# Performance work log

Hardware: AMD Instinct MI355X
Metric: run time of the kernel (lower is better)

## Reference

```python
import jax, jax.numpy as jnp
import numpy as np

N_NODES = 50000
N_EDGES = 1600000
D = 64            # gin_hidden_units == embedding_dim
N_GRAPHS = 512
N_CLASSES = 53
ITERS = 3
VOCAB = 3100
BN_EPS = 1e-5


def setup_inputs() -> dict:
    key = jax.random.key(0)
    ks = jax.random.split(key, 16)
    pkt_length = jax.random.randint(ks[0], (N_NODES,), 0, VOCAB, dtype=jnp.int32)
    src = jax.random.randint(ks[1], (N_EDGES,), 0, N_NODES, dtype=jnp.int32)
    dst = jax.random.randint(ks[2], (N_EDGES,), 0, N_NODES, dtype=jnp.int32)
    graph_ids = jnp.sort(jax.random.randint(ks[3], (N_NODES,), 0, N_GRAPHS, dtype=jnp.int32))
    s = 0.05
    emb = jax.random.normal(ks[4], (VOCAB, D), dtype=jnp.float32) * s
    eps = jnp.zeros((), dtype=jnp.float32)  # GINConv learn_eps init 0
    W1 = jax.random.normal(ks[5], (D, D), dtype=jnp.float32) * s
    b1 = jnp.zeros((D,), dtype=jnp.float32)
    W2 = jax.random.normal(ks[6], (D, D), dtype=jnp.float32) * s
    b2 = jnp.zeros((D,), dtype=jnp.float32)
    W3 = jax.random.normal(ks[7], (D, D), dtype=jnp.float32) * s
    b3 = jnp.zeros((D,), dtype=jnp.float32)
    gamma = jnp.ones((D,), dtype=jnp.float32)
    beta = jnp.zeros((D,), dtype=jnp.float32)
    Wc = jax.random.normal(ks[8], (ITERS * D, N_CLASSES), dtype=jnp.float32) * s
    bc = jnp.zeros((N_CLASSES,), dtype=jnp.float32)
    return {"pkt_length": pkt_length, "src": src, "dst": dst, "graph_ids": graph_ids,
            "emb": emb, "eps": eps, "W1": W1, "b1": b1, "W2": W2, "b2": b2,
            "W3": W3, "b3": b3, "gamma": gamma, "beta": beta, "Wc": Wc, "bc": bc}


def _mlp_bn(x, W1, b1, W2, b2, W3, b3, gamma, beta):
    # 3 Linear+ReLU layers, then BatchNorm1d (training-mode batch stats)
    x = jax.nn.relu(x @ W1 + b1)
    x = jax.nn.relu(x @ W2 + b2)
    x = jax.nn.relu(x @ W3 + b3)
    mean = jnp.mean(x, axis=0)
    var = jnp.var(x, axis=0)
    return gamma * (x - mean) * jax.lax.rsqrt(var + BN_EPS) + beta


def reference(pkt_length, src, dst, graph_ids, emb, eps, W1, b1, W2, b2, W3, b3, gamma, beta, Wc, bc):
    # node features via embedding lookup
    h = emb[pkt_length]  # [N, D]
    pooled = []
    for _ in range(ITERS):
        # GIN sum aggregation: agg[v] = sum_{(u->v)} h[u]
        agg = jax.ops.segment_sum(h[src], dst, num_segments=N_NODES)
        h = _mlp_bn((1.0 + eps) * h + agg, W1, b1, W2, b2, W3, b3, gamma, beta)
        # graph sum pooling
        pooled.append(jax.ops.segment_sum(h, graph_ids, num_segments=N_GRAPHS))
    graph_features = jnp.concatenate(pooled, axis=-1)  # [G, 3*D]
    return graph_features @ Wc + bc  # [G, nb_classes]
```

## Files before the change

### kernel.cpp

```cpp
#include <hip/hip_runtime.h>

#define N_NODES   50000
#define N_EDGES   1600000
#define DDIM      64
#define N_GRAPHS  512
#define N_CLASSES 53
#define ITERS     3
#define NB        782
#define NBLK      391
#define PPITCH    400
#define NPB       128
#define CHUNK     ((N_EDGES + NPB - 1) / NPB)
#define NZERO     (NB + N_GRAPHS)

typedef __bf16 bf16x8 __attribute__((ext_vector_type(8)));
typedef __bf16 bf16x4 __attribute__((ext_vector_type(4)));
typedef float  f32x4  __attribute__((ext_vector_type(4)));

__device__ __forceinline__ float blo16(unsigned w) { return __uint_as_float(w << 16); }
__device__ __forceinline__ float bhi16(unsigned w) { return __uint_as_float(w & 0xffff0000u); }

__global__ void embed_kernel(const int* __restrict__ pkt, const float4* __restrict__ emb,
                             bf16x4* __restrict__ hb4, int* __restrict__ zreg,
                             float* __restrict__ gmbt_id) {
  if (blockIdx.x == 0) {
    for (int i = threadIdx.x; i < NZERO; i += 256) zreg[i] = 0;
    if (threadIdx.x < 128) gmbt_id[threadIdx.x] = (threadIdx.x < 64) ? 1.0f : 0.0f;
  }
  int idx = blockIdx.x * 256 + threadIdx.x;
  if (idx >= N_NODES * 16) return;
  int node = idx >> 4;
  float4 v = emb[(size_t)pkt[node] * 16 + (idx & 15)];
  bf16x4 o;
  o[0] = (__bf16)v.x; o[1] = (__bf16)v.y; o[2] = (__bf16)v.z; o[3] = (__bf16)v.w;
  hb4[idx] = o;
}

__global__ void bucket_hist_kernel(const int* __restrict__ dst, int* __restrict__ bhist) {
  __shared__ int lh[NB];
  for (int i = threadIdx.x; i < NB; i += 256) lh[i] = 0;
  __syncthreads();
  int stride = gridDim.x * 256;
  for (int e = blockIdx.x * 256 + threadIdx.x; e < N_EDGES; e += stride)
    atomicAdd(&lh[dst[e] >> 6], 1);
  __syncthreads();
  for (int i = threadIdx.x; i < NB; i += 256)
    if (lh[i]) atomicAdd(&bhist[i], lh[i]);
}

__global__ void hist_kernel(const int* __restrict__ idx, int* __restrict__ counts, int n) {
  int i = blockIdx.x * 256 + threadIdx.x;
  if (i < n) atomicAdd(&counts[idx[i]], 1);
}

__device__ void scan_body(const int* __restrict__ counts, int* __restrict__ offs,
                          int* __restrict__ cursor, int n) {
  __shared__ int wsum[16];
  __shared__ int carry;
  int tid = threadIdx.x;
  if (tid == 0) carry = 0;
  __syncthreads();
  for (int base = 0; base < n; base += 1024) {
    int i = base + tid;
    int v = (i < n) ? counts[i] : 0;
    int x = v;
    #pragma unroll
    for (int off = 1; off < 64; off <<= 1) {
      int y = __shfl_up(x, off);
      if ((tid & 63) >= off) x += y;
    }
    int w = tid >> 6;
    if ((tid & 63) == 63) wsum[w] = x;
    __syncthreads();
    int woff = 0;
    for (int k = 0; k < w; ++k) woff += wsum[k];
    int incl = x + woff + carry;
    if (i < n) {
      offs[i] = incl - v;
      if (cursor) cursor[i] = incl - v;
    }
    __syncthreads();
    if (tid == 1023) carry = incl;
    __syncthreads();
  }
  if (tid == 0) offs[n] = carry;
}

__global__ void scans_kernel(const int* __restrict__ bhist, int* __restrict__ boffs,
                             int* __restrict__ bcursor, const int* __restrict__ gcnt,
                             int* __restrict__ goff) {
  if (blockIdx.x == 0) scan_body(bhist, boffs, bcursor, NB);
  else                 scan_body(gcnt, goff, nullptr, N_GRAPHS);
}

__global__ __launch_bounds__(1024) void partition_kernel(
    const int* __restrict__ src, const int* __restrict__ dst,
    int* __restrict__ bcursor, unsigned* __restrict__ ebuf) {
  __shared__ int lh[NB];
  __shared__ int lbase[NB];
  for (int i = threadIdx.x; i < NB; i += 1024) lh[i] = 0;
  __syncthreads();
  int e0 = blockIdx.x * CHUNK;
  int e1 = min(e0 + CHUNK, N_EDGES);
  for (int e = e0 + (int)threadIdx.x; e < e1; e += 1024)
    atomicAdd(&lh[dst[e] >> 6], 1);
  __syncthreads();
  for (int i = threadIdx.x; i < NB; i += 1024) {
    int c = lh[i];
    lbase[i] = c ? atomicAdd(&bcursor[i], c) : 0;
    lh[i] = 0;
  }
  __syncthreads();
  for (int e = e0 + (int)threadIdx.x; e < e1; e += 1024) {
    int d = dst[e];
    int b = d >> 6;
    int pos = lbase[b] + atomicAdd(&lh[b], 1);
    ebuf[pos] = (unsigned)src[e] | ((unsigned)(d & 63) << 16);
  }
}

__global__ __launch_bounds__(256) void local_scatter_kernel(
    const unsigned* __restrict__ ebuf, const int* __restrict__ boffs,
    int* __restrict__ offs, int* __restrict__ csr) {
  __shared__ int cnt[64];
  __shared__ int base[64];
  const int b = blockIdx.x;
  const int tid = threadIdx.x;
  if (tid < 64) cnt[tid] = 0;
  __syncthreads();
  const int ebeg = boffs[b], eend = boffs[b + 1];
  for (int e = ebeg + tid; e < eend; e += 256)
    atomicAdd(&cnt[(ebuf[e] >> 16) & 63u], 1);
  __syncthreads();
  if (tid < 64) {
    int v = cnt[tid];
    int x = v;
    #pragma unroll
    for (int off = 1; off < 64; off <<= 1) {
      int y = __shfl_up(x, off);
      if (tid >= off) x += y;
    }
    int excl = ebeg + x - v;
    base[tid] = excl;
    int node = b * 64 + tid;
    if (node < N_NODES) offs[node] = excl;
    cnt[tid] = 0;
  }
  __syncthreads();
  for (int e = ebeg + tid; e < eend; e += 256) {
    unsigned p = ebuf[e];
    int j = (p >> 16) & 63u;
    int pos = base[j] + atomicAdd(&cnt[j], 1);
    csr[pos] = (int)(p & 0xFFFFu);
  }
  if (b == NB - 1 && tid == 0) offs[N_NODES] = N_EDGES;
}

__global__ void pack_weights_kernel(const float* __restrict__ W1, const float* __restrict__ W2,
                                    const float* __restrict__ W3, bf16x8* __restrict__ wbuf) {
  int i = blockIdx.x * 256 + threadIdx.x;
  if (i >= 24 * 64) return;
  int lane = i & 63;
  int frag = i >> 6;
  int t = frag & 3;
  int kc = (frag >> 2) & 1;
  int L = frag >> 3;
  const float* W = (L == 0) ? W1 : ((L == 1) ? W2 : W3);
  int l15 = lane & 15, lg = lane >> 4;
  bf16x8 fh, fl;
  #pragma unroll
  for (int e = 0; e < 8; ++e) {
    int k = kc * 32 + lg * 8 + e;
    float w = W[k * 64 + t * 16 + l15];
    __bf16 hi = (__bf16)w;
    fh[e] = hi;
    fl[e] = (__bf16)(w - (float)hi);
  }
  wbuf[i] = fh;
  wbuf[24 * 64 + i] = fl;
}

__device__ __forceinline__ void split8(const f32x4& v0, const f32x4& v1,
                                       bf16x8& hi, bf16x8& lo) {
  #pragma unroll
  for (int e = 0; e < 4; ++e) {
    __bf16 h0 = (__bf16)v0[e];
    __bf16 h1 = (__bf16)v1[e];
    hi[e] = h0;     lo[e] = (__bf16)(v0[e] - (float)h0);
    hi[4 + e] = h1; lo[4 + e] = (__bf16)(v1[e] - (float)h1);
  }
}

#define MFMA(A, B, C) __builtin_amdgcn_mfma_f32_16x16x32_bf16((A), (B), (C), 0, 0, 0)

#define DOT(L, T, BIASV, ACC)                                        \
  {                                                                  \
    bf16x8 bh0 = wbuf[(((L) * 2 + 0) * 4 + (T)) * 64 + lane];        \
    bf16x8 bh1 = wbuf[(((L) * 2 + 1) * 4 + (T)) * 64 + lane];        \
    bf16x8 bl0 = wbuf[1536 + (((L) * 2 + 0) * 4 + (T)) * 64 + lane]; \
    bf16x8 bl1 = wbuf[1536 + (((L) * 2 + 1) * 4 + (T)) * 64 + lane]; \
    f32x4 a_ = {(BIASV), (BIASV), (BIASV), (BIASV)};                 \
    a_ = MFMA(A0h, bh0, a_);                                         \
    a_ = MFMA(A1h, bh1, a_);                                         \
    a_ = MFMA(A0l, bh0, a_);                                         \
    a_ = MFMA(A1l, bh1, a_);                                         \
    a_ = MFMA(A0h, bl0, a_);                                         \
    a_ = MFMA(A1h, bl1, a_);                                         \
    ACC = a_;                                                        \
  }

#define DOLAYER(L)                   \
  DOT(L, 0, bias##L[0], acc0)        \
  DOT(L, 1, bias##L[1], acc1)        \
  DOT(L, 2, bias##L[2], acc2)        \
  DOT(L, 3, bias##L[3], acc3)

#define STORE_T(T, A)                                         \
  sc[(4 * lg + 0) * 68 + (T) * 16 + l15] = fmaxf(A[0], 0.f);  \
  sc[(4 * lg + 1) * 68 + (T) * 16 + l15] = fmaxf(A[1], 0.f);  \
  sc[(4 * lg + 2) * 68 + (T) * 16 + l15] = fmaxf(A[2], 0.f);  \
  sc[(4 * lg + 3) * 68 + (T) * 16 + l15] = fmaxf(A[3], 0.f);

#define TRANSITION                                            \
  {                                                           \
    STORE_T(0, acc0)                                          \
    STORE_T(1, acc1)                                          \
    STORE_T(2, acc2)                                          \
    STORE_T(3, acc3)                                          \
    const float* rp = sc + l15 * 68 + lg * 8;                 \
    f32x4 r0 = *(const f32x4*)(rp);                           \
    f32x4 r1 = *(const f32x4*)(rp + 4);                       \
    f32x4 r2 = *(const f32x4*)(rp + 32);                      \
    f32x4 r3 = *(const f32x4*)(rp + 36);                      \
    split8(r0, r1, A0h, A0l);                                 \
    split8(r2, r3, A1h, A1l);                                 \
  }

#define EPI_T(T, A)                                                         \
  {                                                                         \
    float v0 = fmaxf(A[0], 0.f), v1 = fmaxf(A[1], 0.f);                     \
    float v2 = fmaxf(A[2], 0.f), v3 = fmaxf(A[3], 0.f);                     \
    if (active) {                                                           \
      xbout[(size_t)(rows0 + 4 * lg + 0) * DDIM + (T) * 16 + l15] = (__bf16)v0; \
      xbout[(size_t)(rows0 + 4 * lg + 1) * DDIM + (T) * 16 + l15] = (__bf16)v1; \
      xbout[(size_t)(rows0 + 4 * lg + 2) * DDIM + (T) * 16 + l15] = (__bf16)v2; \
      xbout[(size_t)(rows0 + 4 * lg + 3) * DDIM + (T) * 16 + l15] = (__bf16)v3; \
    }                                                                       \
    float vs = (v0 + v1) + (v2 + v3);                                       \
    float vq = ((v0 * v0 + v1 * v1) + (v2 * v2 + v3 * v3));                 \
    vs += __shfl_xor(vs, 16); vs += __shfl_xor(vs, 32);                     \
    vq += __shfl_xor(vq, 16); vq += __shfl_xor(vq, 32);                     \
    if (lane < 16) {                                                        \
      bnred[0][wave][(T) * 16 + l15] = vs;                                  \
      bnred[1][wave][(T) * 16 + l15] = vq;                                  \
    }                                                                       \
  }

__global__ __launch_bounds__(512) void agg_mlp_kernel(
    const __bf16* __restrict__ xbin, const int* __restrict__ offs,
    const int* __restrict__ csr, const float* __restrict__ epsp,
    const float* __restrict__ gmbt, __bf16* __restrict__ xbout,
    const bf16x8* __restrict__ wbuf,
    const float* __restrict__ b1, const float* __restrict__ b2,
    const float* __restrict__ b3, float* __restrict__ partial) {
  __shared__ float xt[8 * 16 * 68];
  __shared__ float bnred[2][8][64];
  const int tid = threadIdx.x;
  const int lane = tid & 63, wave = tid >> 6;
  const int l15 = lane & 15, lg = lane >> 4;
  const int rows0 = blockIdx.x * 128 + wave * 16;
  const bool active = rows0 < N_NODES;
  float* xw = xt + wave * (16 * 68);

  {
    const int fl = lane & 7, eg = lane >> 3;
    const uint4* __restrict__ hrow4 = (const uint4*)xbin;
    const float ep = 1.0f + epsp[0];
    f32x4 gA = *(const f32x4*)(gmbt + fl * 8);
    f32x4 gB = *(const f32x4*)(gmbt + fl * 8 + 4);
    f32x4 tA = *(const f32x4*)(gmbt + 64 + fl * 8);
    f32x4 tB = *(const f32x4*)(gmbt + 64 + fl * 8 + 4);
    #pragma unroll
    for (int pass = 0; pass < 2; ++pass) {
      const int node = rows0 + pass * 8 + eg;
      int beg = 0, end = 0;
      if (active) { beg = offs[node]; end = offs[node + 1]; }
      const int deg = end - beg;
      int maxdeg = deg;
      maxdeg = max(maxdeg, __shfl_xor(maxdeg, 8));
      maxdeg = max(maxdeg, __shfl_xor(maxdeg, 16));
      maxdeg = max(maxdeg, __shfl_xor(maxdeg, 32));

      float a0 = 0.f, a1 = 0.f, a2 = 0.f, a3 = 0.f,
            a4 = 0.f, a5 = 0.f, a6 = 0.f, a7 = 0.f;
      if (active) {
        uint4 w = hrow4[(size_t)node * 8 + fl];
        a0 = ep * blo16(w.x); a1 = ep * bhi16(w.x);
        a2 = ep * blo16(w.y); a3 = ep * bhi16(w.y);
        a4 = ep * blo16(w.z); a5 = ep * bhi16(w.z);
        a6 = ep * blo16(w.w); a7 = ep * bhi16(w.w);
      }
      #pragma unroll 4
      for (int it = 0; it < maxdeg; ++it) {
        bool act = it < deg;
        int ci = beg + it;
        ci = (ci < N_EDGES) ? ci : 0;
        int u = csr[ci];
        uint4 w = hrow4[(size_t)u * 8 + fl];
        unsigned m = act ? 0xffffffffu : 0u;
        w.x &= m; w.y &= m; w.z &= m; w.w &= m;
        a0 += blo16(w.x); a1 += bhi16(w.x);
        a2 += blo16(w.y); a3 += bhi16(w.y);
        a4 += blo16(w.z); a5 += bhi16(w.z);
        a6 += blo16(w.w); a7 += bhi16(w.w);
      }
      const float fdeg = ep + (float)deg;
      a0 = fmaf(gA[0], a0, fdeg * tA[0]); a1 = fmaf(gA[1], a1, fdeg * tA[1]);
      a2 = fmaf(gA[2], a2, fdeg * tA[2]); a3 = fmaf(gA[3], a3, fdeg * tA[3]);
      a4 = fmaf(gB[0], a4, fdeg * tB[0]); a5 = fmaf(gB[1], a5, fdeg * tB[1]);
      a6 = fmaf(gB[2], a6, fdeg * tB[2]); a7 = fmaf(gB[3], a7, fdeg * tB[3]);
      float* xp = xw + (pass * 8 + eg) * 68 + fl * 8;
      float4 o0 = {a0, a1, a2, a3};
      float4 o1 = {a4, a5, a6, a7};
      *(float4*)xp = o0;
      *(float4*)(xp + 4) = o1;
    }
  }

  f32x4 acc0 = {0.f, 0.f, 0.f, 0.f}, acc1 = acc0, acc2 = acc0, acc3 = acc0;
  if (active) {
    float bias0[4], bias1[4], bias2[4];
    #pragma unroll
    for (int t = 0; t < 4; ++t) {
      bias0[t] = b1[t * 16 + l15];
      bias1[t] = b2[t * 16 + l15];
      bias2[t] = b3[t * 16 + l15];
    }
    float* sc = xw;
    bf16x8 A0h, A0l, A1h, A1l;
    {
      const float* rp = xw + l15 * 68 + lg * 8;
      f32x4 r0 = *(const f32x4*)(rp);
      f32x4 r1 = *(const f32x4*)(rp + 4);
      f32x4 r2 = *(const f32x4*)(rp + 32);
      f32x4 r3 = *(const f32x4*)(rp + 36);
      split8(r0, r1, A0h, A0l);
      split8(r2, r3, A1h, A1l);
    }
    DOLAYER(0)
    TRANSITION
    DOLAYER(1)
    TRANSITION
    DOLAYER(2)
  }

  EPI_T(0, acc0)
  EPI_T(1, acc1)
  EPI_T(2, acc2)
  EPI_T(3, acc3)

  __syncthreads();
  if (tid < 128) {
    int s = tid >> 6, c = tid & 63;
    float t = 0.f;
    #pragma unroll
    for (int w = 0; w < 8; ++w) t += bnred[s][w][c];
    partial[(size_t)tid * PPITCH + blockIdx.x] = t;
  }
}

__global__ void bn_stats_kernel(const float* __restrict__ partial,
                                const float* __restrict__ gamma,
                                const float* __restrict__ beta,
                                float* __restrict__ gmbt) {
  int d = blockIdx.x * 4 + (threadIdx.x >> 6);
  int lane = threadIdx.x & 63;
  const float* rs = partial + (size_t)d * PPITCH;
  const float* rq = partial + (size_t)(64 + d) * PPITCH;
  float s = 0.f, q = 0.f;
  for (int i = lane; i < NBLK; i += 64) { s += rs[i]; q += rq[i]; }
  #pragma unroll
  for (int off = 32; off > 0; off >>= 1) {
    s += __shfl_down(s, off);
    q += __shfl_down(q, off);
  }
  if (lane == 0) {
    const float invN = 1.0f / N_NODES;
    float mean = s * invN;
    float var = q * invN - mean * mean;
    float gm = gamma[d] / sqrtf(var + 1e-5f);
    gmbt[d] = gm;
    gmbt[64 + d] = beta[d] - mean * gm;
  }
}

__global__ void pool_kernel(const unsigned* __restrict__ xbu, const int* __restrict__ goff,
                            const float* __restrict__ gmbt, float* __restrict__ pooled,
                            int iter) {
  const int g = blockIdx.x;
  const int tid = threadIdx.x;
  const int c = tid & 31;
  const int slot = tid >> 5;
  const int rbeg = goff[g], rend = goff[g + 1];
  float a0 = 0.f, a1 = 0.f;
  for (int r = rbeg + slot; r < rend; r += 8) {
    unsigned w = xbu[(size_t)r * 32 + c];
    a0 += blo16(w);
    a1 += bhi16(w);
  }
  __shared__ float red[8][64];
  red[slot][2 * c] = a0;
  red[slot][2 * c + 1] = a1;
  __syncthreads();
  if (tid < 64) {
    float s = 0.f;
    #pragma unroll
    for (int k = 0; k < 8; ++k) s += red[k][tid];
    float cnt = (float)(rend - rbeg);
    pooled[(size_t)g * (ITERS * DDIM) + iter * DDIM + tid] =
        fmaf(gmbt[tid], s, cnt * gmbt[64 + tid]);
  }
}

__global__ void classifier_kernel(const float* __restrict__ pooled, const float* __restrict__ Wc,
                                  const float* __restrict__ bc, float* __restrict__ out) {
  int g = blockIdx.x;
  int c = threadIdx.x;
  if (c >= N_CLASSES) return;
  float acc = bc[c];
  #pragma unroll 4
  for (int k = 0; k < ITERS * DDIM; ++k)
    acc = fmaf(pooled[(size_t)g * (ITERS * DDIM) + k], Wc[k * N_CLASSES + c], acc);
  out[(size_t)g * N_CLASSES + c] = acc;
}

extern "C" void kernel_launch(void* const* d_in, const int* in_sizes, int n_in,
                              void* d_out, int out_size, void* d_ws, size_t ws_size,
                              hipStream_t stream) {
  const int*   pkt   = (const int*)d_in[0];
  const int*   src   = (const int*)d_in[1];
  const int*   dst   = (const int*)d_in[2];
  const int*   gids  = (const int*)d_in[3];
  const float* emb   = (const float*)d_in[4];
  const float* eps   = (const float*)d_in[5];
  const float* W1    = (const float*)d_in[6];
  const float* b1    = (const float*)d_in[7];
  const float* W2    = (const float*)d_in[8];
  const float* b2    = (const float*)d_in[9];
  const float* W3    = (const float*)d_in[10];
  const float* b3    = (const float*)d_in[11];
  const float* gamma = (const float*)d_in[12];
  const float* beta  = (const float*)d_in[13];
  const float* Wc    = (const float*)d_in[14];
  const float* bc    = (const float*)d_in[15];
  float* out = (float*)d_out;

  char* p = (char*)d_ws;
  auto alloc = [&](size_t bytes) {
    char* r = p;
    p += (bytes + 255) & ~(size_t)255;
    return r;
  };
  __bf16*   hb      = (__bf16*)alloc((size_t)N_NODES * DDIM * 2);
  __bf16*   xb0     = (__bf16*)alloc((size_t)N_NODES * DDIM * 2);
  __bf16*   xb1     = (__bf16*)alloc((size_t)N_NODES * DDIM * 2);
  unsigned* ebuf    = (unsigned*)alloc((size_t)N_EDGES * 4);
  int*      csr     = (int*)alloc((size_t)N_EDGES * 4);
  int*      offs    = (int*)alloc((size_t)(N_NODES + 1) * 4);
  int*      boffs   = (int*)alloc((size_t)(NB + 1) * 4);
  int*      bcursor = (int*)alloc((size_t)NB * 4);
  int*      goff    = (int*)alloc((size_t)(N_GRAPHS + 1) * 4);
  float*    pooled  = (float*)alloc((size_t)N_GRAPHS * ITERS * DDIM * 4);
  float*    gmbt    = (float*)alloc(128 * 4);
  float*    gmbt_id = (float*)alloc(128 * 4);
  bf16x8*   wbuf    = (bf16x8*)alloc((size_t)48 * 64 * 16);
  float*    partial = (float*)alloc((size_t)128 * PPITCH * 4);
  int*   zreg  = (int*)alloc((size_t)NZERO * 4);
  int*   bhist = zreg;
  int*   gcnt  = bhist + NB;

  embed_kernel<<<(N_NODES * 16 + 255) / 256, 256, 0, stream>>>(
      pkt, (const float4*)emb, (bf16x4*)hb, zreg, gmbt_id);
  bucket_hist_kernel<<<512, 256, 0, stream>>>(dst, bhist);
  hist_kernel<<<(N_NODES + 255) / 256, 256, 0, stream>>>(gids, gcnt, N_NODES);
  scans_kernel<<<2, 1024, 0, stream>>>(bhist, boffs, bcursor, gcnt, goff);
  partition_kernel<<<NPB, 1024, 0, stream>>>(src, dst, bcursor, ebuf);
  local_scatter_kernel<<<NB, 256, 0, stream>>>(ebuf, boffs, offs, csr);
  pack_weights_kernel<<<6, 256, 0, stream>>>(W1, W2, W3, wbuf);

  const __bf16* xin[ITERS]  = {hb, xb0, xb1};
  __bf16*       xout[ITERS] = {xb0, xb1, xb0};
  for (int it = 0; it < ITERS; ++it) {
    const float* aff = (it == 0) ? gmbt_id : gmbt;
    agg_mlp_kernel<<<NBLK, 512, 0, stream>>>(xin[it], offs, csr, eps, aff,
                                             xout[it], wbuf, b1, b2, b3, partial);
    bn_stats_kernel<<<16, 256, 0, stream>>>(partial, gamma, beta, gmbt);
    pool_kernel<<<N_GRAPHS, 256, 0, stream>>>((const unsigned*)xout[it], goff,
                                              gmbt, pooled, it);
  }
  classifier_kernel<<<N_GRAPHS, 64, 0, stream>>>(pooled, Wc, bc, out);
}
```

Before: 241.2 us.

## Launch one wave per 16-node tile and write BN partials directly

The fused aggregate+MLP kernel drops from 512-thread blocks covering 128 nodes to 64-thread blocks covering 16 nodes, giving 3125 blocks. The in-block cross-wave BN reduction and its __syncthreads are removed, and each wave writes its sum and sum-of-squares partials straight to global memory. This gives finer-grained scheduling across CUs so waves with high-degree nodes no longer hold back a whole block. The cost is eight times more partials for bn_stats_kernel to reduce. The active-row guards are dropped, which relies on N_NODES being an exact multiple of 16.

```diff
diff --git a/kernel.cpp b/kernel.cpp
--- a/kernel.cpp
+++ b/kernel.cpp
@@ -7,8 +7,8 @@
 #define N_CLASSES 53
 #define ITERS     3
 #define NB        782
-#define NBLK      391
-#define PPITCH    400
+#define NBLK      3125
+#define PPITCH    3200
 #define NPB       128
 #define CHUNK     ((N_EDGES + NPB - 1) / NPB)
 #define NZERO     (NB + N_GRAPHS)
@@ -240,37 +240,32 @@
   {                                                                         \
     float v0 = fmaxf(A[0], 0.f), v1 = fmaxf(A[1], 0.f);                     \
     float v2 = fmaxf(A[2], 0.f), v3 = fmaxf(A[3], 0.f);                     \
-    if (active) {                                                           \
-      xbout[(size_t)(rows0 + 4 * lg + 0) * DDIM + (T) * 16 + l15] = (__bf16)v0; \
-      xbout[(size_t)(rows0 + 4 * lg + 1) * DDIM + (T) * 16 + l15] = (__bf16)v1; \
-      xbout[(size_t)(rows0 + 4 * lg + 2) * DDIM + (T) * 16 + l15] = (__bf16)v2; \
-      xbout[(size_t)(rows0 + 4 * lg + 3) * DDIM + (T) * 16 + l15] = (__bf16)v3; \
-    }                                                                       \
+    xbout[(size_t)(rows0 + 4 * lg + 0) * DDIM + (T) * 16 + l15] = (__bf16)v0; \
+    xbout[(size_t)(rows0 + 4 * lg + 1) * DDIM + (T) * 16 + l15] = (__bf16)v1; \
+    xbout[(size_t)(rows0 + 4 * lg + 2) * DDIM + (T) * 16 + l15] = (__bf16)v2; \
+    xbout[(size_t)(rows0 + 4 * lg + 3) * DDIM + (T) * 16 + l15] = (__bf16)v3; \
     float vs = (v0 + v1) + (v2 + v3);                                       \
     float vq = ((v0 * v0 + v1 * v1) + (v2 * v2 + v3 * v3));                 \
     vs += __shfl_xor(vs, 16); vs += __shfl_xor(vs, 32);                     \
     vq += __shfl_xor(vq, 16); vq += __shfl_xor(vq, 32);                     \
     if (lane < 16) {                                                        \
-      bnred[0][wave][(T) * 16 + l15] = vs;                                  \
-      bnred[1][wave][(T) * 16 + l15] = vq;                                  \
+      partial[(size_t)((T) * 16 + l15) * PPITCH + blk] = vs;                \
+      partial[(size_t)(64 + (T) * 16 + l15) * PPITCH + blk] = vq;           \
     }                                                                       \
   }
 
-__global__ __launch_bounds__(512) void agg_mlp_kernel(
+__global__ __launch_bounds__(64) void agg_mlp_kernel(
     const __bf16* __restrict__ xbin, const int* __restrict__ offs,
     const int* __restrict__ csr, const float* __restrict__ epsp,
     const float* __restrict__ gmbt, __bf16* __restrict__ xbout,
     const bf16x8* __restrict__ wbuf,
     const float* __restrict__ b1, const float* __restrict__ b2,
     const float* __restrict__ b3, float* __restrict__ partial) {
-  __shared__ float xt[8 * 16 * 68];
-  __shared__ float bnred[2][8][64];
-  const int tid = threadIdx.x;
-  const int lane = tid & 63, wave = tid >> 6;
+  __shared__ float xw[16 * 68];
+  const int blk = blockIdx.x;
+  const int lane = threadIdx.x & 63;
   const int l15 = lane & 15, lg = lane >> 4;
-  const int rows0 = blockIdx.x * 128 + wave * 16;
-  const bool active = rows0 < N_NODES;
-  float* xw = xt + wave * (16 * 68);
+  const int rows0 = blk * 16;
 
   {
     const int fl = lane & 7, eg = lane >> 3;
@@ -283,17 +278,15 @@
     #pragma unroll
     for (int pass = 0; pass < 2; ++pass) {
       const int node = rows0 + pass * 8 + eg;
-      int beg = 0, end = 0;
-      if (active) { beg = offs[node]; end = offs[node + 1]; }
+      const int beg = offs[node], end = offs[node + 1];
       const int deg = end - beg;
       int maxdeg = deg;
       maxdeg = max(maxdeg, __shfl_xor(maxdeg, 8));
       maxdeg = max(maxdeg, __shfl_xor(maxdeg, 16));
       maxdeg = max(maxdeg, __shfl_xor(maxdeg, 32));
 
-      float a0 = 0.f, a1 = 0.f, a2 = 0.f, a3 = 0.f,
-            a4 = 0.f, a5 = 0.f, a6 = 0.f, a7 = 0.f;
-      if (active) {
+      float a0, a1, a2, a3, a4, a5, a6, a7;
+      {
         uint4 w = hrow4[(size_t)node * 8 + fl];
         a0 = ep * blo16(w.x); a1 = ep * bhi16(w.x);
         a2 = ep * blo16(w.y); a3 = ep * bhi16(w.y);
@@ -327,8 +320,8 @@
     }
   }
 
-  f32x4 acc0 = {0.f, 0.f, 0.f, 0.f}, acc1 = acc0, acc2 = acc0, acc3 = acc0;
-  if (active) {
+  f32x4 acc0, acc1, acc2, acc3;
+  {
     float bias0[4], bias1[4], bias2[4];
     #pragma unroll
     for (int t = 0; t < 4; ++t) {
@@ -358,15 +351,6 @@
   EPI_T(1, acc1)
   EPI_T(2, acc2)
   EPI_T(3, acc3)
-
-  __syncthreads();
-  if (tid < 128) {
-    int s = tid >> 6, c = tid & 63;
-    float t = 0.f;
-    #pragma unroll
-    for (int w = 0; w < 8; ++w) t += bnred[s][w][c];
-    partial[(size_t)tid * PPITCH + blockIdx.x] = t;
-  }
 }
 
 __global__ void bn_stats_kernel(const float* __restrict__ partial,
@@ -492,8 +476,8 @@
   __bf16*       xout[ITERS] = {xb0, xb1, xb0};
   for (int it = 0; it < ITERS; ++it) {
     const float* aff = (it == 0) ? gmbt_id : gmbt;
-    agg_mlp_kernel<<<NBLK, 512, 0, stream>>>(xin[it], offs, csr, eps, aff,
-                                             xout[it], wbuf, b1, b2, b3, partial);
+    agg_mlp_kernel<<<NBLK, 64, 0, stream>>>(xin[it], offs, csr, eps, aff,
+                                            xout[it], wbuf, b1, b2, b3, partial);
     bn_stats_kernel<<<16, 256, 0, stream>>>(partial, gamma, beta, gmbt);
     pool_kernel<<<N_GRAPHS, 256, 0, stream>>>((const unsigned*)xout[it], goff,
                                               gmbt, pooled, it);
```

Result: slower. 278.5 us (+15.5%).
